# Kernel optimization log

Hardware: AMD Instinct MI355X
Metric: run time of the kernel (lower is better)

Reference implementation:

```python
import jax, jax.numpy as jnp
import numpy as np

D_MODEL = 1024
NHEAD = 16
D_K = D_MODEL // NHEAD


def setup_inputs() -> dict:
    key = jax.random.key(0)
    ks = jax.random.split(key, 8)
    B, S = 2, 2048
    scale = 1.0 / np.sqrt(D_MODEL)
    return {
        "Q": jax.random.normal(ks[0], (B, S, D_MODEL), dtype=jnp.float32),
        "K": jax.random.normal(ks[1], (B, S, D_MODEL), dtype=jnp.float32),
        "V": jax.random.normal(ks[2], (B, S, D_MODEL), dtype=jnp.float32),
        "WQ": jax.random.normal(ks[3], (D_MODEL, D_MODEL), dtype=jnp.float32) * scale,
        "WK": jax.random.normal(ks[4], (D_MODEL, D_MODEL), dtype=jnp.float32) * scale,
        "WV": jax.random.normal(ks[5], (D_MODEL, D_MODEL), dtype=jnp.float32) * scale,
        "Wfc": jax.random.normal(ks[6], (D_MODEL, D_MODEL), dtype=jnp.float32) * scale,
        "bfc": jax.random.normal(ks[7], (D_MODEL,), dtype=jnp.float32) * 0.01,
    }


def reference(Q, K, V, WQ, WK, WV, Wfc, bfc):
    B, Sq, _ = Q.shape
    Skv = K.shape[1]
    # Linear projections (torch Linear: x @ W^T), split into heads: [B, H, S, d_k]
    q = (Q @ WQ.T).reshape(B, Sq, NHEAD, D_K).transpose(0, 2, 1, 3)
    k = (K @ WK.T).reshape(B, Skv, NHEAD, D_K).transpose(0, 2, 1, 3)
    v = (V @ WV.T).reshape(B, Skv, NHEAD, D_K).transpose(0, 2, 1, 3)
    # Scaled dot-product scores: [B, H, Sq, Skv]
    scores = jnp.einsum("bhqd,bhkd->bhqk", q, k) / jnp.sqrt(jnp.float32(D_K))
    # Causal mask (strict upper triangle -> -inf)
    causal = jnp.tril(jnp.ones((Sq, Skv), dtype=bool))
    scores = jnp.where(causal, scores, -jnp.inf)
    attn = jax.nn.softmax(scores, axis=-1)
    y = jnp.einsum("bhqk,bhkd->bhqd", attn, v)
    y = y.transpose(0, 2, 1, 3).reshape(B, Sq, D_MODEL)
    return y @ Wfc.T + bfc
```

## Files before the change

kernel.cpp:

```cpp
#include <hip/hip_runtime.h>

typedef __attribute__((ext_vector_type(8))) short bf16x8;
typedef __attribute__((ext_vector_type(4))) float f32x4;
typedef __attribute__((ext_vector_type(16))) float f32x16;

__device__ __forceinline__ ushort f2bf(float f) {
    union { float f; unsigned u; } x; x.f = f;
    unsigned r = x.u + 0x7fffu + ((x.u >> 16) & 1u);
    return (ushort)(r >> 16);
}

__device__ __forceinline__ void async16(const void* g, void* l) {
    __builtin_amdgcn_global_load_lds(
        (const __attribute__((address_space(1))) void*)g,
        (__attribute__((address_space(3))) void*)l, 16, 0, 0);
}

__device__ __forceinline__ f32x4 mfma16(bf16x8 a, bf16x8 b, f32x4 c) {
    return __builtin_amdgcn_mfma_f32_16x16x32_bf16(a, b, c, 0, 0, 0);
}
__device__ __forceinline__ f32x16 mfma32(bf16x8 a, bf16x8 b, f32x16 c) {
    return __builtin_amdgcn_mfma_f32_32x32x16_bf16(a, b, c, 0, 0, 0);
}

__device__ __forceinline__ f32x4 zero4() { f32x4 z = {0.f, 0.f, 0.f, 0.f}; return z; }

__global__ void cvt7_kernel(
    const float* __restrict__ s0, const float* __restrict__ s1, const float* __restrict__ s2,
    const float* __restrict__ s3, const float* __restrict__ s4, const float* __restrict__ s5,
    const float* __restrict__ s6,
    ushort* __restrict__ d0, ushort* __restrict__ d1, ushort* __restrict__ d2,
    ushort* __restrict__ d3, ushort* __restrict__ d4, ushort* __restrict__ d5,
    ushort* __restrict__ d6)
{
    int y = blockIdx.y;
    const float* s; ushort* d; int n4;
    if      (y == 0) { s = s0; d = d0; n4 = 1048576; }
    else if (y == 1) { s = s1; d = d1; n4 = 1048576; }
    else if (y == 2) { s = s2; d = d2; n4 = 1048576; }
    else if (y == 3) { s = s3; d = d3; n4 = 262144; }
    else if (y == 4) { s = s4; d = d4; n4 = 262144; }
    else if (y == 5) { s = s5; d = d5; n4 = 262144; }
    else             { s = s6; d = d6; n4 = 262144; }
    int i = blockIdx.x * 256 + threadIdx.x;
    if (i >= n4) return;
    float4 v = ((const float4*)s)[i];
    ushort4 o;
    o.x = f2bf(v.x); o.y = f2bf(v.y); o.z = f2bf(v.z); o.w = f2bf(v.w);
    ((ushort4*)d)[i] = o;
}

template<bool SWAP>
__device__ __forceinline__ void gemm_core(
    const ushort* __restrict__ A, const ushort* __restrict__ W,
    char* smem, int bm, int bn, int tid, f32x4 acc[4][4])
{
    const int lane = tid & 63;
    const int wid  = tid >> 6;
    const int wr = wid >> 1, wc = wid & 1;
    const int l15 = lane & 15, g = lane >> 4;

    auto stage = [&](int kt, int b) {
        char* As = smem + b * 32768;
        char* Bs = As + 16384;
        #pragma unroll
        for (int it = 0; it < 4; ++it) {
            int c = it * 256 + tid;
            int row = c >> 3;
            int inner = c & 7;
            int srcoff = (inner ^ (row & 7)) * 16;
            async16((const char*)A + (size_t)(bm * 128 + row) * 2048 + kt * 128 + srcoff, As + c * 16);
            async16((const char*)W + (size_t)(bn * 128 + row) * 2048 + kt * 128 + srcoff, Bs + c * 16);
        }
    };

    stage(0, 0);
    __syncthreads();

    for (int kt = 0; kt < 16; ++kt) {
        const int cur = kt & 1;
        if (kt < 15) stage(kt + 1, cur ^ 1);

        const char* As = smem + cur * 32768;
        const char* Bs = As + 16384;
        bf16x8 af[4][2], bfr[4][2];
        #pragma unroll
        for (int mt = 0; mt < 4; ++mt)
            #pragma unroll
            for (int ks = 0; ks < 2; ++ks) {
                int row = wr * 64 + mt * 16 + l15;
                int byte = (row * 128 + ks * 64 + g * 16) ^ ((row & 7) << 4);
                af[mt][ks] = *(const bf16x8*)(As + byte);
            }
        #pragma unroll
        for (int nt = 0; nt < 4; ++nt)
            #pragma unroll
            for (int ks = 0; ks < 2; ++ks) {
                int row = wc * 64 + nt * 16 + l15;
                int byte = (row * 128 + ks * 64 + g * 16) ^ ((row & 7) << 4);
                bfr[nt][ks] = *(const bf16x8*)(Bs + byte);
            }
        #pragma unroll
        for (int mt = 0; mt < 4; ++mt)
            #pragma unroll
            for (int nt = 0; nt < 4; ++nt) {
                if (SWAP) {
                    acc[mt][nt] = mfma16(bfr[nt][0], af[mt][0], acc[mt][nt]);
                    acc[mt][nt] = mfma16(bfr[nt][1], af[mt][1], acc[mt][nt]);
                } else {
                    acc[mt][nt] = mfma16(af[mt][0], bfr[nt][0], acc[mt][nt]);
                    acc[mt][nt] = mfma16(af[mt][1], bfr[nt][1], acc[mt][nt]);
                }
            }
        __syncthreads();
    }
}

__global__ __launch_bounds__(256) void gemm_qkv(
    const ushort* __restrict__ Qb, const ushort* __restrict__ Kb, const ushort* __restrict__ Vb,
    const ushort* __restrict__ WQ, const ushort* __restrict__ WK, const ushort* __restrict__ WV,
    ushort* __restrict__ qhb, ushort* __restrict__ khb, ushort* __restrict__ vhT)
{
    __shared__ __align__(16) char smem[65536];
    const int tid = threadIdx.x;
    const int z  = blockIdx.x % 3;
    const int bm = blockIdx.x / 3;
    const int bn = blockIdx.y;
    const int lane = tid & 63;
    const int wid  = tid >> 6;
    const int wr = wid >> 1, wc = wid & 1;
    const int l15 = lane & 15, g = lane >> 4;

    const ushort* A  = (z == 0) ? Qb : (z == 1) ? Kb : Vb;
    const ushort* Wm = (z == 0) ? WQ : (z == 1) ? WK : WV;

    f32x4 acc[4][4];
    #pragma unroll
    for (int i = 0; i < 4; ++i)
        #pragma unroll
        for (int j = 0; j < 4; ++j) acc[i][j] = zero4();

    if (z == 2) {
        gemm_core<true>(A, Wm, smem, bm, bn, tid, acc);
        #pragma unroll
        for (int mt = 0; mt < 4; ++mt)
            #pragma unroll
            for (int nt = 0; nt < 4; ++nt)
                #pragma unroll
                for (int j = 0; j < 4; ++j) {
                    int n = bn * 128 + wc * 64 + nt * 16 + g * 4 + j;
                    int m = bm * 128 + wr * 64 + mt * 16 + l15;
                    int b = m >> 11, s = m & 2047, h = (n >> 6) & 15, d = n & 63;
                    vhT[(((size_t)(b * 16 + h)) * 64 + d) * 2048 + s] = f2bf(acc[mt][nt][j]);
                }
    } else {
        gemm_core<false>(A, Wm, smem, bm, bn, tid, acc);
        const float scale = (z == 0) ? 0.125f : 1.0f;
        ushort* outb = (z == 0) ? qhb : khb;
        #pragma unroll
        for (int mt = 0; mt < 4; ++mt)
            #pragma unroll
            for (int nt = 0; nt < 4; ++nt)
                #pragma unroll
                for (int j = 0; j < 4; ++j) {
                    int m = bm * 128 + wr * 64 + mt * 16 + g * 4 + j;
                    int n = bn * 128 + wc * 64 + nt * 16 + l15;
                    int b = m >> 11, s = m & 2047, h = n >> 6, d = n & 63;
                    outb[(((size_t)(b * 16 + h)) * 2048 + s) * 64 + d] = f2bf(acc[mt][nt][j] * scale);
                }
    }
}

__global__ __launch_bounds__(256) void gemm_fc(
    const ushort* __restrict__ A, const ushort* __restrict__ W,
    float* __restrict__ outf, const float* __restrict__ bias)
{
    __shared__ __align__(16) char smem[65536];
    const int tid = threadIdx.x;
    const int lane = tid & 63;
    const int wid  = tid >> 6;
    const int wr = wid >> 1, wc = wid & 1;
    const int l15 = lane & 15, g = lane >> 4;

    f32x4 acc[4][4];
    #pragma unroll
    for (int i = 0; i < 4; ++i)
        #pragma unroll
        for (int j = 0; j < 4; ++j) acc[i][j] = zero4();

    gemm_core<false>(A, W, smem, blockIdx.x, blockIdx.y, tid, acc);

    #pragma unroll
    for (int mt = 0; mt < 4; ++mt)
        #pragma unroll
        for (int nt = 0; nt < 4; ++nt)
            #pragma unroll
            for (int j = 0; j < 4; ++j) {
                int m = blockIdx.x * 128 + wr * 64 + mt * 16 + g * 4 + j;
                int n = blockIdx.y * 128 + wc * 64 + nt * 16 + l15;
                outf[(size_t)m * 1024 + n] = acc[mt][nt][j] + bias[n];
            }
}

__global__ __launch_bounds__(256, 2) void attn_kernel(
    const ushort* __restrict__ qh, const ushort* __restrict__ kh,
    const ushort* __restrict__ vhT, ushort* __restrict__ yb)
{
    __shared__ __align__(16) char smem[32768];
    const int tid = threadIdx.x;
    const int lane = tid & 63, wid = tid >> 6;
    const int l31 = lane & 31;
    const int hi  = lane >> 5;
    const int bh = blockIdx.y;
    const int qt = (bh < 16) ? (int)blockIdx.x : 15 - (int)blockIdx.x;
    const int q0 = qt * 128;
    const size_t base = (size_t)bh * 2048 * 64;
    const int qrw = q0 + wid * 32;

    auto stageK = [&](int t, int b) {
        char* Ks = smem + b * 8192;
        #pragma unroll
        for (int it = 0; it < 2; ++it) {
            int c = it * 256 + tid;
            int row = c >> 3, inner = c & 7;
            async16((const char*)kh + (base + (size_t)(t * 64 + row) * 64) * 2 + ((inner ^ (row & 7)) * 16),
                    Ks + c * 16);
        }
    };
    auto stageV = [&](int t, int b) {
        char* Vs = smem + 16384 + b * 8192;
        #pragma unroll
        for (int it = 0; it < 2; ++it) {
            int c = it * 256 + tid;
            int row = c >> 3, inner = c & 7;
            async16((const char*)vhT + (base + (size_t)row * 2048 + (size_t)t * 64) * 2 + ((inner ^ (row & 7)) * 16),
                    Vs + c * 16);
        }
    };

    bf16x8 qf[4];
    #pragma unroll
    for (int ks = 0; ks < 4; ++ks)
        qf[ks] = *(const bf16x8*)((const char*)qh + (base + (size_t)(qrw + l31) * 64) * 2 + ks * 32 + hi * 16);

    f32x16 o[2];
    #pragma unroll
    for (int r = 0; r < 16; ++r) { o[0][r] = 0.f; o[1][r] = 0.f; }
    float m_run = -1e30f, l_run = 0.f;

    const int nkv = qt * 2 + 2;
    stageK(0, 0); stageV(0, 0);
    __syncthreads();

    for (int t = 0; t < nkv; ++t) {
        const int kv0 = t * 64;
        const int cur = t & 1;
        if (t + 1 < nkv) { stageK(t + 1, cur ^ 1); stageV(t + 1, cur ^ 1); }

        if (kv0 <= qrw + 31) {
            const char* Ks = smem + cur * 8192;
            const char* Vs = smem + 16384 + cur * 8192;

            f32x16 st[2];
            #pragma unroll
            for (int r = 0; r < 16; ++r) { st[0][r] = 0.f; st[1][r] = 0.f; }
            #pragma unroll
            for (int tt = 0; tt < 2; ++tt)
                #pragma unroll
                for (int ks = 0; ks < 4; ++ks) {
                    int row = tt * 32 + l31;
                    int byte = (row * 128 + ks * 32 + hi * 16) ^ ((row & 7) << 4);
                    bf16x8 kf = *(const bf16x8*)(Ks + byte);
                    st[tt] = mfma32(kf, qf[ks], st[tt]);
                }

            if (kv0 + 63 > qrw) {
                #pragma unroll
                for (int tt = 0; tt < 2; ++tt)
                    #pragma unroll
                    for (int r = 0; r < 16; ++r) {
                        int kv = kv0 + tt * 32 + (r & 3) + 8 * (r >> 2) + 4 * hi;
                        if (kv > qrw + l31) st[tt][r] = -1e30f;
                    }
            }

            float mx = st[0][0];
            #pragma unroll
            for (int tt = 0; tt < 2; ++tt)
                #pragma unroll
                for (int r = 0; r < 16; ++r) mx = fmaxf(mx, st[tt][r]);
            mx = fmaxf(mx, __shfl_xor(mx, 32));

            if (!__all(mx - m_run <= 8.0f)) {
                float mn = fmaxf(m_run, mx);
                float corr = __expf(m_run - mn);
                l_run *= corr;
                m_run = mn;
                #pragma unroll
                for (int r = 0; r < 16; ++r) {
                    int qsrc = (r & 3) + 8 * (r >> 2) + 4 * hi;
                    float c2 = __shfl(corr, qsrc);
                    o[0][r] *= c2; o[1][r] *= c2;
                }
            }

            float sum = 0.f;
            #pragma unroll
            for (int tt = 0; tt < 2; ++tt)
                #pragma unroll
                for (int r = 0; r < 16; ++r) {
                    float p = __expf(st[tt][r] - m_run);
                    st[tt][r] = p;
                    sum += p;
                }
            sum += __shfl_xor(sum, 32);
            l_run += sum;

            unsigned Wd[2][8], Xw[2][8];
            #pragma unroll
            for (int tt = 0; tt < 2; ++tt)
                #pragma unroll
                for (int k = 0; k < 8; ++k) {
                    unsigned w;
                    asm("v_cvt_pk_bf16_f32 %0, %1, %2" : "=v"(w) : "v"(st[tt][2 * k]), "v"(st[tt][2 * k + 1]));
                    Wd[tt][k] = w;
                }
            #pragma unroll
            for (int tt = 0; tt < 2; ++tt)
                #pragma unroll
                for (int k = 0; k < 8; ++k)
                    Xw[tt][k] = __shfl_xor((int)Wd[tt][k], 32);

            #pragma unroll
            for (int ks = 0; ks < 4; ++ks) {
                const int t2 = ks >> 1, bse = (ks & 1) * 4;
                unsigned w0 = hi ? Xw[t2][bse + 2] : Wd[t2][bse + 0];
                unsigned w1 = hi ? Xw[t2][bse + 3] : Wd[t2][bse + 1];
                unsigned w2 = hi ? Wd[t2][bse + 2] : Xw[t2][bse + 0];
                unsigned w3 = hi ? Wd[t2][bse + 3] : Xw[t2][bse + 1];
                unsigned pw[4] = {w0, w1, w2, w3};
                bf16x8 pf = *(const bf16x8*)pw;
                #pragma unroll
                for (int dt = 0; dt < 2; ++dt) {
                    int row = dt * 32 + l31;
                    int byte = (row * 128 + ks * 32 + hi * 16) ^ ((row & 7) << 4);
                    bf16x8 vf = *(const bf16x8*)(Vs + byte);
                    o[dt] = mfma32(pf, vf, o[dt]);
                }
            }
        }
        __syncthreads();
    }

    const int b = bh >> 4, h = bh & 15;
    float invl = 1.0f / l_run;
    #pragma unroll
    for (int r = 0; r < 16; ++r) {
        int qsrc = (r & 3) + 8 * (r >> 2) + 4 * hi;
        float iv = __shfl(invl, qsrc);
        int q = qrw + qsrc;
        size_t rowoff = ((size_t)(b * 2048 + q)) * 1024 + h * 64;
        yb[rowoff + l31]      = f2bf(o[0][r] * iv);
        yb[rowoff + 32 + l31] = f2bf(o[1][r] * iv);
    }
}

extern "C" void kernel_launch(void* const* d_in, const int* in_sizes, int n_in,
                              void* d_out, int out_size, void* d_ws, size_t ws_size,
                              hipStream_t stream)
{
    const size_t MD = 4096ull * 1024;
    const size_t WD = 1024ull * 1024;
    ushort* ws  = (ushort*)d_ws;
    ushort* Qb  = ws;
    ushort* Kb  = Qb + MD;
    ushort* Vb  = Kb + MD;
    ushort* qhb = Vb + MD;
    ushort* khb = qhb + MD;
    ushort* vhT = khb + MD;
    ushort* WQb = vhT + MD;
    ushort* WKb = WQb + WD;
    ushort* WVb = WKb + WD;
    ushort* Wfb = WVb + WD;
    ushort* yb  = Qb;

    cvt7_kernel<<<dim3(4096, 7), 256, 0, stream>>>(
        (const float*)d_in[0], (const float*)d_in[1], (const float*)d_in[2],
        (const float*)d_in[3], (const float*)d_in[4], (const float*)d_in[5],
        (const float*)d_in[6],
        Qb, Kb, Vb, WQb, WKb, WVb, Wfb);

    gemm_qkv<<<dim3(96, 8), 256, 0, stream>>>(Qb, Kb, Vb, WQb, WKb, WVb, qhb, khb, vhT);
    attn_kernel<<<dim3(16, 32), 256, 0, stream>>>(qhb, khb, vhT, yb);
    gemm_fc<<<dim3(32, 8), 256, 0, stream>>>(yb, Wfb, (float*)d_out, (const float*)d_in[7]);
}
```

Baseline: 121.1 us.

## Split attention KV across two wave groups and shrink QKV GEMM K-tile

The attention kernel now runs 512 threads in two wave groups. Each group handles half of a 128-wide KV tile for the same 128 query rows, and the groups' partial softmax states (o, m, l) are merged through shared memory at the end. This doubles the waves available per query tile so latency is hidden better, and s_setprio is placed around the MFMA sections. The QKV GEMM uses a K-tile of 32 with half the LDS, raising occupancy, at the cost of more loop iterations and barriers; the FC GEMM keeps a K-tile of 64.

```diff
diff --git a/kernel.cpp b/kernel.cpp
--- a/kernel.cpp
+++ b/kernel.cpp
@@ -50,68 +50,82 @@
     ((ushort4*)d)[i] = o;
 }
 
-template<bool SWAP>
+template<bool SWAP, int BK>
 __device__ __forceinline__ void gemm_core(
     const ushort* __restrict__ A, const ushort* __restrict__ W,
     char* smem, int bm, int bn, int tid, f32x4 acc[4][4])
 {
+    constexpr int TILEB = 128 * BK * 2;
+    constexpr int NSTEP = 1024 / BK;
     const int lane = tid & 63;
     const int wid  = tid >> 6;
     const int wr = wid >> 1, wc = wid & 1;
     const int l15 = lane & 15, g = lane >> 4;
 
     auto stage = [&](int kt, int b) {
-        char* As = smem + b * 32768;
-        char* Bs = As + 16384;
-        #pragma unroll
-        for (int it = 0; it < 4; ++it) {
-            int c = it * 256 + tid;
-            int row = c >> 3;
-            int inner = c & 7;
-            int srcoff = (inner ^ (row & 7)) * 16;
-            async16((const char*)A + (size_t)(bm * 128 + row) * 2048 + kt * 128 + srcoff, As + c * 16);
-            async16((const char*)W + (size_t)(bn * 128 + row) * 2048 + kt * 128 + srcoff, Bs + c * 16);
+        char* As = smem + b * (2 * TILEB);
+        char* Bs = As + TILEB;
+        if (BK == 64) {
+            #pragma unroll
+            for (int it = 0; it < 4; ++it) {
+                int c = it * 256 + tid;
+                int row = c >> 3, inner = c & 7;
+                int srcoff = (inner ^ (row & 7)) * 16;
+                async16((const char*)A + (size_t)(bm * 128 + row) * 2048 + kt * 128 + srcoff, As + c * 16);
+                async16((const char*)W + (size_t)(bn * 128 + row) * 2048 + kt * 128 + srcoff, Bs + c * 16);
+            }
+        } else {
+            #pragma unroll
+            for (int it = 0; it < 2; ++it) {
+                int c = it * 256 + tid;
+                int row = c >> 2, inner = c & 3;
+                int srcoff = (inner ^ (row & 3)) * 16;
+                async16((const char*)A + (size_t)(bm * 128 + row) * 2048 + kt * 64 + srcoff, As + c * 16);
+                async16((const char*)W + (size_t)(bn * 128 + row) * 2048 + kt * 64 + srcoff, Bs + c * 16);
+            }
         }
     };
 
     stage(0, 0);
     __syncthreads();
 
-    for (int kt = 0; kt < 16; ++kt) {
+    for (int kt = 0; kt < NSTEP; ++kt) {
         const int cur = kt & 1;
-        if (kt < 15) stage(kt + 1, cur ^ 1);
-
-        const char* As = smem + cur * 32768;
-        const char* Bs = As + 16384;
-        bf16x8 af[4][2], bfr[4][2];
+        if (kt < NSTEP - 1) stage(kt + 1, cur ^ 1);
+
+        const char* As = smem + cur * (2 * TILEB);
+        const char* Bs = As + TILEB;
+        constexpr int KS = BK / 32;
+        bf16x8 af[4][KS], bfr[4][KS];
         #pragma unroll
         for (int mt = 0; mt < 4; ++mt)
             #pragma unroll
-            for (int ks = 0; ks < 2; ++ks) {
+            for (int ks = 0; ks < KS; ++ks) {
                 int row = wr * 64 + mt * 16 + l15;
-                int byte = (row * 128 + ks * 64 + g * 16) ^ ((row & 7) << 4);
+                int byte;
+                if (BK == 64) byte = (row * 128 + ks * 64 + g * 16) ^ ((row & 7) << 4);
+                else          byte = (row * 64 + g * 16) ^ ((row & 3) << 4);
                 af[mt][ks] = *(const bf16x8*)(As + byte);
             }
         #pragma unroll
         for (int nt = 0; nt < 4; ++nt)
             #pragma unroll
-            for (int ks = 0; ks < 2; ++ks) {
+            for (int ks = 0; ks < KS; ++ks) {
                 int row = wc * 64 + nt * 16 + l15;
-                int byte = (row * 128 + ks * 64 + g * 16) ^ ((row & 7) << 4);
+                int byte;
+                if (BK == 64) byte = (row * 128 + ks * 64 + g * 16) ^ ((row & 7) << 4);
+                else          byte = (row * 64 + g * 16) ^ ((row & 3) << 4);
                 bfr[nt][ks] = *(const bf16x8*)(Bs + byte);
             }
         #pragma unroll
         for (int mt = 0; mt < 4; ++mt)
             #pragma unroll
-            for (int nt = 0; nt < 4; ++nt) {
-                if (SWAP) {
-                    acc[mt][nt] = mfma16(bfr[nt][0], af[mt][0], acc[mt][nt]);
-                    acc[mt][nt] = mfma16(bfr[nt][1], af[mt][1], acc[mt][nt]);
-                } else {
-                    acc[mt][nt] = mfma16(af[mt][0], bfr[nt][0], acc[mt][nt]);
-                    acc[mt][nt] = mfma16(af[mt][1], bfr[nt][1], acc[mt][nt]);
-                }
-            }
+            for (int nt = 0; nt < 4; ++nt)
+                #pragma unroll
+                for (int ks = 0; ks < KS; ++ks) {
+                    if (SWAP) acc[mt][nt] = mfma16(bfr[nt][ks], af[mt][ks], acc[mt][nt]);
+                    else      acc[mt][nt] = mfma16(af[mt][ks], bfr[nt][ks], acc[mt][nt]);
+                }
         __syncthreads();
     }
 }
@@ -121,7 +135,7 @@
     const ushort* __restrict__ WQ, const ushort* __restrict__ WK, const ushort* __restrict__ WV,
     ushort* __restrict__ qhb, ushort* __restrict__ khb, ushort* __restrict__ vhT)
 {
-    __shared__ __align__(16) char smem[65536];
+    __shared__ __align__(16) char smem[32768];
     const int tid = threadIdx.x;
     const int z  = blockIdx.x % 3;
     const int bm = blockIdx.x / 3;
@@ -141,7 +155,7 @@
         for (int j = 0; j < 4; ++j) acc[i][j] = zero4();
 
     if (z == 2) {
-        gemm_core<true>(A, Wm, smem, bm, bn, tid, acc);
+        gemm_core<true, 32>(A, Wm, smem, bm, bn, tid, acc);
         #pragma unroll
         for (int mt = 0; mt < 4; ++mt)
             #pragma unroll
@@ -154,7 +168,7 @@
                     vhT[(((size_t)(b * 16 + h)) * 64 + d) * 2048 + s] = f2bf(acc[mt][nt][j]);
                 }
     } else {
-        gemm_core<false>(A, Wm, smem, bm, bn, tid, acc);
+        gemm_core<false, 32>(A, Wm, smem, bm, bn, tid, acc);
         const float scale = (z == 0) ? 0.125f : 1.0f;
         ushort* outb = (z == 0) ? qhb : khb;
         #pragma unroll
@@ -188,7 +202,7 @@
         #pragma unroll
         for (int j = 0; j < 4; ++j) acc[i][j] = zero4();
 
-    gemm_core<false>(A, W, smem, blockIdx.x, blockIdx.y, tid, acc);
+    gemm_core<false, 64>(A, W, smem, blockIdx.x, blockIdx.y, tid, acc);
 
     #pragma unroll
     for (int mt = 0; mt < 4; ++mt)
@@ -202,38 +216,40 @@
             }
 }
 
-__global__ __launch_bounds__(256, 2) void attn_kernel(
+__global__ __launch_bounds__(512, 4) void attn_kernel(
     const ushort* __restrict__ qh, const ushort* __restrict__ kh,
     const ushort* __restrict__ vhT, ushort* __restrict__ yb)
 {
-    __shared__ __align__(16) char smem[32768];
+    __shared__ __align__(16) char smem[65536];
     const int tid = threadIdx.x;
     const int lane = tid & 63, wid = tid >> 6;
     const int l31 = lane & 31;
     const int hi  = lane >> 5;
+    const int group = wid >> 2;
+    const int wq    = wid & 3;
+    const int subkv = group * 64;
     const int bh = blockIdx.y;
     const int qt = (bh < 16) ? (int)blockIdx.x : 15 - (int)blockIdx.x;
-    const int q0 = qt * 128;
     const size_t base = (size_t)bh * 2048 * 64;
-    const int qrw = q0 + wid * 32;
+    const int qrw = qt * 128 + wq * 32;
 
     auto stageK = [&](int t, int b) {
-        char* Ks = smem + b * 8192;
+        char* Ks = smem + b * 16384;
         #pragma unroll
         for (int it = 0; it < 2; ++it) {
-            int c = it * 256 + tid;
+            int c = it * 512 + tid;
             int row = c >> 3, inner = c & 7;
-            async16((const char*)kh + (base + (size_t)(t * 64 + row) * 64) * 2 + ((inner ^ (row & 7)) * 16),
+            async16((const char*)kh + (base + (size_t)(t * 128 + row) * 64) * 2 + ((inner ^ (row & 7)) * 16),
                     Ks + c * 16);
         }
     };
     auto stageV = [&](int t, int b) {
-        char* Vs = smem + 16384 + b * 8192;
+        char* Vs = smem + 32768 + b * 16384;
         #pragma unroll
         for (int it = 0; it < 2; ++it) {
-            int c = it * 256 + tid;
-            int row = c >> 3, inner = c & 7;
-            async16((const char*)vhT + (base + (size_t)row * 2048 + (size_t)t * 64) * 2 + ((inner ^ (row & 7)) * 16),
+            int c = it * 512 + tid;
+            int row = c >> 4, inner = c & 15;
+            async16((const char*)vhT + (base + (size_t)row * 2048 + (size_t)t * 128) * 2 + ((inner ^ (row & 15)) * 16),
                     Vs + c * 16);
         }
     };
@@ -248,31 +264,32 @@
     for (int r = 0; r < 16; ++r) { o[0][r] = 0.f; o[1][r] = 0.f; }
     float m_run = -1e30f, l_run = 0.f;
 
-    const int nkv = qt * 2 + 2;
     stageK(0, 0); stageV(0, 0);
     __syncthreads();
 
-    for (int t = 0; t < nkv; ++t) {
-        const int kv0 = t * 64;
-        const int cur = t & 1;
-        if (t + 1 < nkv) { stageK(t + 1, cur ^ 1); stageV(t + 1, cur ^ 1); }
-
+    for (int i = 0; i <= qt; ++i) {
+        const int cur = i & 1;
+        if (i < qt) { stageK(i + 1, cur ^ 1); stageV(i + 1, cur ^ 1); }
+
+        const int kv0 = i * 128 + subkv;
         if (kv0 <= qrw + 31) {
-            const char* Ks = smem + cur * 8192;
-            const char* Vs = smem + 16384 + cur * 8192;
+            const char* Ks = smem + cur * 16384;
+            const char* Vs = smem + 32768 + cur * 16384;
 
             f32x16 st[2];
             #pragma unroll
             for (int r = 0; r < 16; ++r) { st[0][r] = 0.f; st[1][r] = 0.f; }
+            __builtin_amdgcn_s_setprio(1);
             #pragma unroll
             for (int tt = 0; tt < 2; ++tt)
                 #pragma unroll
                 for (int ks = 0; ks < 4; ++ks) {
-                    int row = tt * 32 + l31;
-                    int byte = (row * 128 + ks * 32 + hi * 16) ^ ((row & 7) << 4);
+                    int krow = subkv + tt * 32 + l31;
+                    int byte = (krow * 128 + ks * 32 + hi * 16) ^ ((krow & 7) << 4);
                     bf16x8 kf = *(const bf16x8*)(Ks + byte);
                     st[tt] = mfma32(kf, qf[ks], st[tt]);
                 }
+            __builtin_amdgcn_s_setprio(0);
 
             if (kv0 + 63 > qrw) {
                 #pragma unroll
@@ -340,28 +357,52 @@
                 unsigned w3 = hi ? Wd[t2][bse + 3] : Xw[t2][bse + 1];
                 unsigned pw[4] = {w0, w1, w2, w3};
                 bf16x8 pf = *(const bf16x8*)pw;
+                __builtin_amdgcn_s_setprio(1);
                 #pragma unroll
                 for (int dt = 0; dt < 2; ++dt) {
-                    int row = dt * 32 + l31;
-                    int byte = (row * 128 + ks * 32 + hi * 16) ^ ((row & 7) << 4);
+                    int vrow = dt * 32 + l31;
+                    int colB = subkv * 2 + ks * 32 + hi * 16;
+                    int byte = vrow * 256 + (colB ^ ((vrow & 15) << 4));
                     bf16x8 vf = *(const bf16x8*)(Vs + byte);
                     o[dt] = mfma32(pf, vf, o[dt]);
                 }
+                __builtin_amdgcn_s_setprio(0);
             }
         }
         __syncthreads();
     }
 
-    const int b = bh >> 4, h = bh & 15;
-    float invl = 1.0f / l_run;
-    #pragma unroll
-    for (int r = 0; r < 16; ++r) {
-        int qsrc = (r & 3) + 8 * (r >> 2) + 4 * hi;
-        float iv = __shfl(invl, qsrc);
-        int q = qrw + qsrc;
-        size_t rowoff = ((size_t)(b * 2048 + q)) * 1024 + h * 64;
-        yb[rowoff + l31]      = f2bf(o[0][r] * iv);
-        yb[rowoff + 32 + l31] = f2bf(o[1][r] * iv);
+    float* oml = (float*)smem;
+    if (group == 1) {
+        float* p = oml + (size_t)(wq * 64 + lane) * 36;
+        #pragma unroll
+        for (int r = 0; r < 16; ++r) { p[r] = o[0][r]; p[16 + r] = o[1][r]; }
+        p[32] = m_run; p[33] = l_run;
+    }
+    __syncthreads();
+    if (group == 0) {
+        const float* p = oml + (size_t)(wq * 64 + lane) * 36;
+        float m1 = p[32], l1 = p[33];
+        float mn = fmaxf(m_run, m1);
+        float a0 = __expf(m_run - mn);
+        float a1 = __expf(m1 - mn);
+        float lt = l_run * a0 + l1 * a1;
+        float invl = 1.0f / lt;
+
+        const int b = bh >> 4, h = bh & 15;
+        #pragma unroll
+        for (int r = 0; r < 16; ++r) {
+            int qsrc = (r & 3) + 8 * (r >> 2) + 4 * hi;
+            float f0 = __shfl(a0, qsrc);
+            float f1 = __shfl(a1, qsrc);
+            float iv = __shfl(invl, qsrc);
+            float v0 = (o[0][r] * f0 + p[r] * f1) * iv;
+            float v1 = (o[1][r] * f0 + p[16 + r] * f1) * iv;
+            int q = qrw + qsrc;
+            size_t rowoff = ((size_t)(b * 2048 + q)) * 1024 + h * 64;
+            yb[rowoff + l31]      = f2bf(v0);
+            yb[rowoff + 32 + l31] = f2bf(v1);
+        }
     }
 }
 
@@ -391,6 +432,6 @@
         Qb, Kb, Vb, WQb, WKb, WVb, Wfb);
 
     gemm_qkv<<<dim3(96, 8), 256, 0, stream>>>(Qb, Kb, Vb, WQb, WKb, WVb, qhb, khb, vhT);
-    attn_kernel<<<dim3(16, 32), 256, 0, stream>>>(qhb, khb, vhT, yb);
+    attn_kernel<<<dim3(16, 32), 512, 0, stream>>>(qhb, khb, vhT, yb);
     gemm_fc<<<dim3(32, 8), 256, 0, stream>>>(yb, Wfb, (float*)d_out, (const float*)d_in[7]);
 }
```

Result: no change. 121.8 us (+0.5%).
